# Kernel optimization log

Hardware: AMD Instinct MI355X
Metric: run time of the kernel (lower is better)

Reference implementation:

```python
import jax, jax.numpy as jnp
import numpy as np

B, K, T, H, D = 16, 49, 256, 512, 512


def setup_inputs() -> dict:
    key = jax.random.key(0)
    ks = jax.random.split(key, 8)
    s = 1.0 / np.sqrt(H)
    return {
        "V": jax.random.normal(ks[0], (B, K, H), jnp.float32),
        "h_t": jax.random.normal(ks[1], (B, T, H), jnp.float32),
        "s_t": jax.random.normal(ks[2], (B, T, H), jnp.float32),
        "Wv": jax.random.normal(ks[3], (H, D), jnp.float32) * s,
        "bv": jnp.zeros((D,), jnp.float32),
        "Wg": jax.random.normal(ks[4], (H, D), jnp.float32) * s,
        "bg": jnp.zeros((D,), jnp.float32),
        "Ws": jax.random.normal(ks[5], (H, D), jnp.float32) * s,
        "bs": jnp.zeros((D,), jnp.float32),
        "Wh": jax.random.normal(ks[6], (D, 1), jnp.float32) * (1.0 / np.sqrt(D)),
        "bh": jnp.zeros((1,), jnp.float32),
    }


def reference(V, h_t, s_t, Wv, bv, Wg, bg, Ws, bs, Wh, bh):
    # projections (dropout is identity in eval)
    cv = V @ Wv + bv                        # [B, K, D]
    cg = h_t @ Wg + bg                      # [B, T, D]
    # content_v: [B, T, K, D] via broadcast add
    content_v = cv[:, None, :, :] + cg[:, :, None, :]
    z_t = (jnp.tanh(content_v) @ Wh + bh)[..., 0]   # [B, T, K]
    alpha_t = jax.nn.softmax(z_t, axis=-1)          # [B, T, K]
    c_t = jnp.einsum('btk,bkh->bth', alpha_t, V)    # [B, T, H]
    # sentinel branch
    content_s = (s_t @ Ws + bs) + cg                # [B, T, D]
    z_ext = jnp.tanh(content_s) @ Wh + bh           # [B, T, 1]
    extended = jnp.concatenate([z_t, z_ext], axis=-1)  # [B, T, K+1]
    alpha_hat = jax.nn.softmax(extended, axis=-1)
    beta_t = alpha_hat[:, :, -1:]                   # [B, T, 1]
    c_hat_t = beta_t * s_t + (1.0 - beta_t) * c_t   # [B, T, H]
    return (c_hat_t, alpha_t, beta_t)
```

## Files before the change

kernel.cpp:

```cpp
#include <hip/hip_runtime.h>
#include <hip/hip_fp16.h>
#include <cstdint>
#include <cstddef>

#define B_ 16
#define K_ 49
#define T_ 256
#define H_ 512
#define D_ 512

#define TANH_SCALE 2.8853900817779268f
#define LOG2E 1.4426950408889634f

typedef _Float16 half8 __attribute__((ext_vector_type(8)));
typedef float floatx4 __attribute__((ext_vector_type(4)));

#define ROWS_A 9088
#define OFF_V 0
#define OFF_H 896
#define OFF_S 4992

__global__ __launch_bounds__(256) void conv_a(const float* __restrict__ V,
                                              const float* __restrict__ h_t,
                                              const float* __restrict__ s_t,
                                              _Float16* __restrict__ Af16) {
    int idx = (blockIdx.x * 256 + threadIdx.x) * 8;
    int row = idx >> 9;
    int col = idx & 511;
    const float* src;
    if (row < 784)        src = V   + (size_t)row * 512 + col;
    else if (row < 896)   src = nullptr;
    else if (row < 4992)  src = h_t + (size_t)(row - 896) * 512 + col;
    else                  src = s_t + (size_t)(row - 4992) * 512 + col;

    half8 h;
    if (src) {
        float4 f0 = *(const float4*)(src);
        float4 f1 = *(const float4*)(src + 4);
        h[0] = (_Float16)f0.x; h[1] = (_Float16)f0.y;
        h[2] = (_Float16)f0.z; h[3] = (_Float16)f0.w;
        h[4] = (_Float16)f1.x; h[5] = (_Float16)f1.y;
        h[6] = (_Float16)f1.z; h[7] = (_Float16)f1.w;
    } else {
        h = (half8)((_Float16)0.0f);
    }
    *(half8*)(Af16 + idx) = h;
}

__global__ __launch_bounds__(256) void conv_w(const float* __restrict__ Wv,
                                              const float* __restrict__ Wg,
                                              const float* __restrict__ Ws,
                                              _Float16* __restrict__ Wt) {
    int p = blockIdx.z;
    const float* W = (p == 0) ? Wv : (p == 1) ? Wg : Ws;
    _Float16* outp = Wt + (size_t)p * 512 * 512;
    __shared__ float tile[32][33];
    int tx = threadIdx.x, ty = threadIdx.y;
    int c = blockIdx.x * 32 + tx;
    int rbase = blockIdx.y * 32;
#pragma unroll
    for (int i = 0; i < 4; i++)
        tile[ty + i * 8][tx] = W[(size_t)(rbase + ty + i * 8) * 512 + c];
    __syncthreads();
    int k = rbase + tx;
#pragma unroll
    for (int i = 0; i < 4; i++) {
        int n = blockIdx.x * 32 + ty + i * 8;
        outp[(size_t)n * 512 + k] = (_Float16)(tile[tx][ty + i * 8] * TANH_SCALE);
    }
}

#define GS 56
__global__ __launch_bounds__(256) void gemm_f16(
    const _Float16* __restrict__ Af16, const _Float16* __restrict__ Wt,
    const float* __restrict__ bv, const float* __restrict__ bg2,
    const float* __restrict__ bs, float* __restrict__ cv,
    float* __restrict__ cg, float* __restrict__ cs) {
    __shared__ __align__(16) _Float16 As[128 * GS];
    __shared__ __align__(16) _Float16 Bs[128 * GS];

    int id = blockIdx.x;
    int rowbase; const _Float16* Bt; const float* bias; float* C;
    if (id < 28)        { rowbase = OFF_V; Bt = Wt;            bias = bv;  C = cv; }
    else if (id < 156)  { id -= 28;  rowbase = OFF_H; Bt = Wt + 262144; bias = bg2; C = cg; }
    else                { id -= 156; rowbase = OFF_S; Bt = Wt + 524288; bias = bs;  C = cs; }
    int tm = id >> 2, tn = id & 3;

    int tid = threadIdx.x;
    int wave = tid >> 6, lane = tid & 63;
    int wm = wave >> 1, wn = wave & 1;

    int sr = tid >> 1;
    int sc = (tid & 1) << 4;
    const _Float16* ag  = Af16 + (size_t)(rowbase + tm * 128 + sr) * 512 + sc;
    const _Float16* bgp = Bt   + (size_t)(tn * 128 + sr) * 512 + sc;
    _Float16* asw = &As[sr * GS + sc];
    _Float16* bsw = &Bs[sr * GS + sc];

    int fm = lane & 15, q = lane >> 4;
    const _Float16* ar = &As[(wm * 64 + fm) * GS + q * 8];
    const _Float16* br = &Bs[(wn * 64 + fm) * GS + q * 8];

    floatx4 acc[4][4];
#pragma unroll
    for (int x = 0; x < 4; x++)
#pragma unroll
        for (int y = 0; y < 4; y++) acc[x][y] = (floatx4)0.0f;

    for (int kk = 0; kk < 16; kk++) {
        if (kk) __syncthreads();
        int4 a0 = *(const int4*)(ag);
        int4 a1 = *(const int4*)(ag + 8);
        int4 b0 = *(const int4*)(bgp);
        int4 b1 = *(const int4*)(bgp + 8);
        ag += 32; bgp += 32;
        *(int4*)(asw)     = a0;
        *(int4*)(asw + 8) = a1;
        *(int4*)(bsw)     = b0;
        *(int4*)(bsw + 8) = b1;
        __syncthreads();

        half8 af[4], bf[4];
#pragma unroll
        for (int x = 0; x < 4; x++) af[x] = *(const half8*)(ar + x * 16 * GS);
#pragma unroll
        for (int y = 0; y < 4; y++) bf[y] = *(const half8*)(br + y * 16 * GS);
#pragma unroll
        for (int x = 0; x < 4; x++)
#pragma unroll
            for (int y = 0; y < 4; y++)
                acc[x][y] = __builtin_amdgcn_mfma_f32_16x16x32_f16(af[x], bf[y], acc[x][y], 0, 0, 0);
    }

    int dn = lane & 15, dq = lane >> 4;
#pragma unroll
    for (int x = 0; x < 4; x++) {
        int rowg = tm * 128 + wm * 64 + x * 16 + dq * 4;
#pragma unroll
        for (int y = 0; y < 4; y++) {
            int colg = tn * 128 + wn * 64 + y * 16 + dn;
            float bc = bias[colg] * TANH_SCALE;
#pragma unroll
            for (int r = 0; r < 4; r++)
                C[(size_t)(rowg + r) * 512 + colg] = acc[x][y][r] + bc;
        }
    }
}

__device__ __forceinline__ float wave_sum(float v) {
#pragma unroll
    for (int o = 32; o > 0; o >>= 1) v += __shfl_xor(v, o);
    return v;
}
__device__ __forceinline__ float wave_max(float v) {
#pragma unroll
    for (int o = 32; o > 0; o >>= 1) v = fmaxf(v, __shfl_xor(v, o));
    return v;
}

#define TB 4
__global__ __launch_bounds__(256) void z_kernel(
    const float* __restrict__ cv, const float* __restrict__ cg,
    const float* __restrict__ cs, const float* __restrict__ V,
    const float* __restrict__ s_t, const float* __restrict__ Wh,
    const float* __restrict__ bh, float* __restrict__ out) {
    int bx = blockIdx.x;
    int b  = bx >> 6;
    int t0 = (bx & 63) << 2;
    int bt0 = b * 256 + t0;
    int tid = threadIdx.x;
    int wave = tid >> 6, lane = tid & 63;

    __shared__ float zl[TB][64];
    __shared__ float4 al4[52];
    __shared__ float bl[TB];

    float whv[8], cgv[TB][8];
#pragma unroll
    for (int j = 0; j < 8; j++) whv[j] = Wh[j * 64 + lane];
#pragma unroll
    for (int tt = 0; tt < TB; tt++) {
        const float* cgp = cg + (size_t)(bt0 + tt) * 512;
#pragma unroll
        for (int j = 0; j < 8; j++) cgv[tt][j] = cgp[j * 64 + lane];
    }
    float s8 = 0.0f;
#pragma unroll
    for (int j = 0; j < 8; j++) s8 += whv[j];
    float zbase = wave_sum(s8) + bh[0];

    for (int task = wave; task < 49; task += 4) {
        const float* rp = cv + (size_t)(b * 49 + task) * 512;
        float rv[8];
#pragma unroll
        for (int j = 0; j < 8; j++) rv[j] = rp[j * 64 + lane];
        float acc[TB] = {0.0f, 0.0f, 0.0f, 0.0f};
#pragma unroll
        for (int tt = 0; tt < TB; tt++) {
#pragma unroll
            for (int j = 0; j < 8; j++) {
                float x = rv[j] + cgv[tt][j];
                float e = __builtin_amdgcn_exp2f(x);
                float r = __builtin_amdgcn_rcpf(1.0f + e);
                acc[tt] = fmaf(whv[j], r, acc[tt]);
            }
        }
#pragma unroll
        for (int tt = 0; tt < TB; tt++) {
            float s = wave_sum(acc[tt]);
            if (lane == 0) zl[tt][task] = zbase - 2.0f * s;
        }
    }
#pragma unroll
    for (int tt = 0; tt < TB; tt++) {
        if (wave == tt) {
            const float* rp = cs + (size_t)(bt0 + tt) * 512;
            float acc = 0.0f;
#pragma unroll
            for (int j = 0; j < 8; j++) {
                float x = rp[j * 64 + lane] + cgv[tt][j];
                float e = __builtin_amdgcn_exp2f(x);
                float r = __builtin_amdgcn_rcpf(1.0f + e);
                acc = fmaf(whv[j], r, acc);
            }
            float s = wave_sum(acc);
            if (lane == 0) zl[tt][49] = zbase - 2.0f * s;
        }
    }
    __syncthreads();

    {
        int w = wave;
        float z = (lane < 49) ? zl[w][lane] : -3.0e38f;
        float m = wave_max(z);
        float e = (lane < 49) ? __builtin_amdgcn_exp2f((z - m) * LOG2E) : 0.0f;
        float s = wave_sum(e);
        float zext = zl[w][49];
        float m2 = fmaxf(m, zext);
        float sc   = __builtin_amdgcn_exp2f((m - m2) * LOG2E);
        float eext = __builtin_amdgcn_exp2f((zext - m2) * LOG2E);
        float s2 = s * sc + eext;
        float beta = eext / s2;
        if (lane < 49) {
            float a = e / s;
            ((float*)&al4[lane])[w] = a;
            out[(size_t)B_ * T_ * H_ + (size_t)(bt0 + w) * 49 + lane] = a;
        }
        if (lane == 0) {
            bl[w] = beta;
            out[(size_t)B_ * T_ * H_ + (size_t)B_ * T_ * K_ + (bt0 + w)] = beta;
        }
    }
    __syncthreads();

    const float* Vb = V + (size_t)b * 49 * 512;
    float acc1[TB] = {0, 0, 0, 0}, acc2[TB] = {0, 0, 0, 0};
    for (int k = 0; k < 49; k++) {
        float4 a4 = al4[k];
        float v1 = Vb[(size_t)k * 512 + tid];
        float v2 = Vb[(size_t)k * 512 + 256 + tid];
        acc1[0] = fmaf(a4.x, v1, acc1[0]);  acc2[0] = fmaf(a4.x, v2, acc2[0]);
        acc1[1] = fmaf(a4.y, v1, acc1[1]);  acc2[1] = fmaf(a4.y, v2, acc2[1]);
        acc1[2] = fmaf(a4.z, v1, acc1[2]);  acc2[2] = fmaf(a4.z, v2, acc2[2]);
        acc1[3] = fmaf(a4.w, v1, acc1[3]);  acc2[3] = fmaf(a4.w, v2, acc2[3]);
    }
#pragma unroll
    for (int tt = 0; tt < TB; tt++) {
        float beta = bl[tt];
        const float* sp = s_t + (size_t)(bt0 + tt) * 512;
        out[(size_t)(bt0 + tt) * 512 + tid]       = beta * sp[tid]       + (1.0f - beta) * acc1[tt];
        out[(size_t)(bt0 + tt) * 512 + 256 + tid] = beta * sp[tid + 256] + (1.0f - beta) * acc2[tt];
    }
}

extern "C" void kernel_launch(void* const* d_in, const int* in_sizes, int n_in,
                              void* d_out, int out_size, void* d_ws, size_t ws_size,
                              hipStream_t stream) {
    const float* V   = (const float*)d_in[0];
    const float* h_t = (const float*)d_in[1];
    const float* s_t = (const float*)d_in[2];
    const float* Wv  = (const float*)d_in[3];
    const float* bv  = (const float*)d_in[4];
    const float* Wg  = (const float*)d_in[5];
    const float* bg  = (const float*)d_in[6];
    const float* Ws  = (const float*)d_in[7];
    const float* bs  = (const float*)d_in[8];
    const float* Wh  = (const float*)d_in[9];
    const float* bh  = (const float*)d_in[10];
    float* out = (float*)d_out;

    char* ws = (char*)d_ws;
    _Float16* Af16 = (_Float16*)(ws);
    _Float16* Wt   = (_Float16*)(ws + 9306112);
    float* cv = (float*)(ws + 10878976);
    float* cg = (float*)(ws + 12713984);
    float* cs = (float*)(ws + 21102592);

    conv_a<<<2272, 256, 0, stream>>>(V, h_t, s_t, Af16);
    conv_w<<<dim3(16, 16, 3), dim3(32, 8), 0, stream>>>(Wv, Wg, Ws, Wt);
    gemm_f16<<<284, 256, 0, stream>>>(Af16, Wt, bv, bg, bs, cv, cg, cs);
    z_kernel<<<1024, 256, 0, stream>>>(cv, cg, cs, V, s_t, Wh, bh, out);
}
```

Baseline: 143.0 us.

## Merge conversion kernels, retile GEMM with async LDS loads, overlap z_kernel loads

Folds the activation and weight fp16 conversion kernels into one launch to save a kernel launch. The GEMM moves to 64x128 tiles with twice as many blocks, loads K=64 per stage through global_load_lds into a pre-swizzled fragment layout, and each wave now covers a 64x32 output slice. In z_kernel the next cv row is prefetched into registers, the four per-row wave reductions are replaced by a combined butterfly reduction, and the alpha·V loop is unrolled. Smaller tiles raise occupancy across CUs but reduce data reuse per block.

Result: no change. 140.6 us (-1.7%).

```diff
diff --git a/kernel.cpp b/kernel.cpp
--- a/kernel.cpp
+++ b/kernel.cpp
@@ -20,125 +20,141 @@
 #define OFF_H 896
 #define OFF_S 4992
 
-__global__ __launch_bounds__(256) void conv_a(const float* __restrict__ V,
-                                              const float* __restrict__ h_t,
-                                              const float* __restrict__ s_t,
-                                              _Float16* __restrict__ Af16) {
-    int idx = (blockIdx.x * 256 + threadIdx.x) * 8;
-    int row = idx >> 9;
-    int col = idx & 511;
-    const float* src;
-    if (row < 784)        src = V   + (size_t)row * 512 + col;
-    else if (row < 896)   src = nullptr;
-    else if (row < 4992)  src = h_t + (size_t)(row - 896) * 512 + col;
-    else                  src = s_t + (size_t)(row - 4992) * 512 + col;
-
-    half8 h;
-    if (src) {
-        float4 f0 = *(const float4*)(src);
-        float4 f1 = *(const float4*)(src + 4);
-        h[0] = (_Float16)f0.x; h[1] = (_Float16)f0.y;
-        h[2] = (_Float16)f0.z; h[3] = (_Float16)f0.w;
-        h[4] = (_Float16)f1.x; h[5] = (_Float16)f1.y;
-        h[6] = (_Float16)f1.z; h[7] = (_Float16)f1.w;
+__device__ __forceinline__ void async16(const _Float16* g, const _Float16* l) {
+    __builtin_amdgcn_global_load_lds(
+        (const __attribute__((address_space(1))) unsigned int*)g,
+        (__attribute__((address_space(3))) unsigned int*)l, 16, 0, 0);
+}
+
+__global__ __launch_bounds__(256) void conv_all(const float* __restrict__ V,
+                                                const float* __restrict__ h_t,
+                                                const float* __restrict__ s_t,
+                                                const float* __restrict__ Wv,
+                                                const float* __restrict__ Wg,
+                                                const float* __restrict__ Ws,
+                                                _Float16* __restrict__ Af16,
+                                                _Float16* __restrict__ Wt) {
+    __shared__ float tile[32][33];
+    int tid = threadIdx.x;
+    if (blockIdx.x < 2272) {
+        int idx = (blockIdx.x * 256 + tid) * 8;
+        int row = idx >> 9;
+        int col = idx & 511;
+        const float* src;
+        if (row < 784)        src = V   + (size_t)row * 512 + col;
+        else if (row < 896)   src = nullptr;
+        else if (row < 4992)  src = h_t + (size_t)(row - 896) * 512 + col;
+        else                  src = s_t + (size_t)(row - 4992) * 512 + col;
+        half8 h;
+        if (src) {
+            float4 f0 = *(const float4*)(src);
+            float4 f1 = *(const float4*)(src + 4);
+            h[0] = (_Float16)f0.x; h[1] = (_Float16)f0.y;
+            h[2] = (_Float16)f0.z; h[3] = (_Float16)f0.w;
+            h[4] = (_Float16)f1.x; h[5] = (_Float16)f1.y;
+            h[6] = (_Float16)f1.z; h[7] = (_Float16)f1.w;
+        } else {
+            h = (half8)((_Float16)0.0f);
+        }
+        *(half8*)(Af16 + idx) = h;
     } else {
-        h = (half8)((_Float16)0.0f);
-    }
-    *(half8*)(Af16 + idx) = h;
-}
-
-__global__ __launch_bounds__(256) void conv_w(const float* __restrict__ Wv,
-                                              const float* __restrict__ Wg,
-                                              const float* __restrict__ Ws,
-                                              _Float16* __restrict__ Wt) {
-    int p = blockIdx.z;
-    const float* W = (p == 0) ? Wv : (p == 1) ? Wg : Ws;
-    _Float16* outp = Wt + (size_t)p * 512 * 512;
-    __shared__ float tile[32][33];
-    int tx = threadIdx.x, ty = threadIdx.y;
-    int c = blockIdx.x * 32 + tx;
-    int rbase = blockIdx.y * 32;
-#pragma unroll
-    for (int i = 0; i < 4; i++)
-        tile[ty + i * 8][tx] = W[(size_t)(rbase + ty + i * 8) * 512 + c];
-    __syncthreads();
-    int k = rbase + tx;
-#pragma unroll
-    for (int i = 0; i < 4; i++) {
-        int n = blockIdx.x * 32 + ty + i * 8;
-        outp[(size_t)n * 512 + k] = (_Float16)(tile[tx][ty + i * 8] * TANH_SCALE);
-    }
-}
-
-#define GS 56
+        int bid = blockIdx.x - 2272;
+        int p = bid >> 8;
+        int rem = bid & 255;
+        int bx = rem & 15, by = rem >> 4;
+        const float* W = (p == 0) ? Wv : (p == 1) ? Wg : Ws;
+        _Float16* outp = Wt + (size_t)p * 512 * 512;
+        int tx = tid & 31, ty = tid >> 5;
+        int c = bx * 32 + tx;
+        int rbase = by * 32;
+#pragma unroll
+        for (int i = 0; i < 4; i++)
+            tile[ty + i * 8][tx] = W[(size_t)(rbase + ty + i * 8) * 512 + c];
+        __syncthreads();
+        int k = rbase + tx;
+#pragma unroll
+        for (int i = 0; i < 4; i++) {
+            int n = bx * 32 + ty + i * 8;
+            outp[(size_t)n * 512 + k] = (_Float16)(tile[tx][ty + i * 8] * TANH_SCALE);
+        }
+    }
+}
+
 __global__ __launch_bounds__(256) void gemm_f16(
     const _Float16* __restrict__ Af16, const _Float16* __restrict__ Wt,
     const float* __restrict__ bv, const float* __restrict__ bg2,
     const float* __restrict__ bs, float* __restrict__ cv,
     float* __restrict__ cg, float* __restrict__ cs) {
-    __shared__ __align__(16) _Float16 As[128 * GS];
-    __shared__ __align__(16) _Float16 Bs[128 * GS];
+    __shared__ __align__(16) _Float16 As[64 * 64];
+    __shared__ __align__(16) _Float16 Bs[128 * 64];
 
     int id = blockIdx.x;
     int rowbase; const _Float16* Bt; const float* bias; float* C;
-    if (id < 28)        { rowbase = OFF_V; Bt = Wt;            bias = bv;  C = cv; }
-    else if (id < 156)  { id -= 28;  rowbase = OFF_H; Bt = Wt + 262144; bias = bg2; C = cg; }
-    else                { id -= 156; rowbase = OFF_S; Bt = Wt + 524288; bias = bs;  C = cs; }
+    if (id < 56)        { rowbase = OFF_V;            Bt = Wt;          bias = bv;  C = cv; }
+    else if (id < 312)  { id -= 56;  rowbase = OFF_H; Bt = Wt + 262144; bias = bg2; C = cg; }
+    else                { id -= 312; rowbase = OFF_S; Bt = Wt + 524288; bias = bs;  C = cs; }
     int tm = id >> 2, tn = id & 3;
 
     int tid = threadIdx.x;
     int wave = tid >> 6, lane = tid & 63;
-    int wm = wave >> 1, wn = wave & 1;
-
-    int sr = tid >> 1;
-    int sc = (tid & 1) << 4;
-    const _Float16* ag  = Af16 + (size_t)(rowbase + tm * 128 + sr) * 512 + sc;
-    const _Float16* bgp = Bt   + (size_t)(tn * 128 + sr) * 512 + sc;
-    _Float16* asw = &As[sr * GS + sc];
-    _Float16* bsw = &Bs[sr * GS + sc];
-
-    int fm = lane & 15, q = lane >> 4;
-    const _Float16* ar = &As[(wm * 64 + fm) * GS + q * 8];
-    const _Float16* br = &Bs[(wn * 64 + fm) * GS + q * 8];
-
-    floatx4 acc[4][4];
+
+    const _Float16* gA[2];
+    int ldsA[2];
+#pragma unroll
+    for (int i = 0; i < 2; i++) {
+        int p = i * 256 + tid;
+        int ks = p >> 8, x = (p >> 6) & 3, q = (p >> 4) & 3, fm = p & 15;
+        gA[i] = Af16 + (size_t)(rowbase + tm * 64 + x * 16 + fm) * 512 + ks * 32 + q * 8;
+        ldsA[i] = p * 8;
+    }
+    const _Float16* gB[4];
+    int ldsB[4];
+#pragma unroll
+    for (int i = 0; i < 4; i++) {
+        int p = i * 256 + tid;
+        int ks = p >> 9, w2y = (p >> 6) & 7, q = (p >> 4) & 3, fn = p & 15;
+        gB[i] = Bt + (size_t)(tn * 128 + w2y * 16 + fn) * 512 + ks * 32 + q * 8;
+        ldsB[i] = p * 8;
+    }
+
+    floatx4 acc[4][2];
 #pragma unroll
     for (int x = 0; x < 4; x++)
 #pragma unroll
-        for (int y = 0; y < 4; y++) acc[x][y] = (floatx4)0.0f;
-
-    for (int kk = 0; kk < 16; kk++) {
+        for (int y = 0; y < 2; y++) acc[x][y] = (floatx4)0.0f;
+
+    for (int kk = 0; kk < 8; kk++) {
         if (kk) __syncthreads();
-        int4 a0 = *(const int4*)(ag);
-        int4 a1 = *(const int4*)(ag + 8);
-        int4 b0 = *(const int4*)(bgp);
-        int4 b1 = *(const int4*)(bgp + 8);
-        ag += 32; bgp += 32;
-        *(int4*)(asw)     = a0;
-        *(int4*)(asw + 8) = a1;
-        *(int4*)(bsw)     = b0;
-        *(int4*)(bsw + 8) = b1;
+#pragma unroll
+        for (int i = 0; i < 2; i++) async16(gA[i] + kk * 64, &As[ldsA[i]]);
+#pragma unroll
+        for (int i = 0; i < 4; i++) async16(gB[i] + kk * 64, &Bs[ldsB[i]]);
         __syncthreads();
 
-        half8 af[4], bf[4];
-#pragma unroll
-        for (int x = 0; x < 4; x++) af[x] = *(const half8*)(ar + x * 16 * GS);
-#pragma unroll
-        for (int y = 0; y < 4; y++) bf[y] = *(const half8*)(br + y * 16 * GS);
-#pragma unroll
-        for (int x = 0; x < 4; x++)
-#pragma unroll
-            for (int y = 0; y < 4; y++)
-                acc[x][y] = __builtin_amdgcn_mfma_f32_16x16x32_f16(af[x], bf[y], acc[x][y], 0, 0, 0);
+#pragma unroll
+        for (int ks = 0; ks < 2; ks++) {
+            half8 a[4], bf[2];
+#pragma unroll
+            for (int x = 0; x < 4; x++)
+                a[x] = *(const half8*)&As[((ks * 4 + x) * 64 + lane) * 8];
+#pragma unroll
+            for (int y = 0; y < 2; y++)
+                bf[y] = *(const half8*)&Bs[((ks * 8 + wave * 2 + y) * 64 + lane) * 8];
+#pragma unroll
+            for (int x = 0; x < 4; x++)
+#pragma unroll
+                for (int y = 0; y < 2; y++)
+                    acc[x][y] = __builtin_amdgcn_mfma_f32_16x16x32_f16(a[x], bf[y], acc[x][y], 0, 0, 0);
+        }
     }
 
     int dn = lane & 15, dq = lane >> 4;
 #pragma unroll
     for (int x = 0; x < 4; x++) {
-        int rowg = tm * 128 + wm * 64 + x * 16 + dq * 4;
-#pragma unroll
-        for (int y = 0; y < 4; y++) {
-            int colg = tn * 128 + wn * 64 + y * 16 + dn;
+        int rowg = tm * 64 + x * 16 + dq * 4;
+#pragma unroll
+        for (int y = 0; y < 2; y++) {
+            int colg = tn * 128 + wave * 32 + y * 16 + dn;
             float bc = bias[colg] * TANH_SCALE;
 #pragma unroll
             for (int r = 0; r < 4; r++)
@@ -156,6 +172,25 @@
 #pragma unroll
     for (int o = 32; o > 0; o >>= 1) v = fmaxf(v, __shfl_xor(v, o));
     return v;
+}
+
+__device__ __forceinline__ float xsum4(float a0, float a1, float a2, float a3, int lane) {
+    bool hi = (lane & 32) != 0;
+    float t0 = hi ? a0 : a2;
+    float t1 = hi ? a1 : a3;
+    t0 = __shfl_xor(t0, 32);
+    t1 = __shfl_xor(t1, 32);
+    if (hi) { a0 = t0; a1 = t1; } else { a2 = t0; a3 = t1; }
+    bool h2 = (lane & 16) != 0;
+    float u0 = h2 ? a0 : a1;
+    float u1 = h2 ? a2 : a3;
+    u0 = __shfl_xor(u0, 16);
+    u1 = __shfl_xor(u1, 16);
+    if (h2) { a0 = u0; a2 = u1; } else { a1 = u0; a3 = u1; }
+    float s = (a0 + a1) + (a2 + a3);
+#pragma unroll
+    for (int o = 8; o > 0; o >>= 1) s += __shfl_xor(s, o);
+    return s;
 }
 
 #define TB 4
@@ -189,11 +224,19 @@
     for (int j = 0; j < 8; j++) s8 += whv[j];
     float zbase = wave_sum(s8) + bh[0];
 
+    float rv[8], rn[8];
+    {
+        const float* rp = cv + (size_t)(b * 49 + wave) * 512;
+#pragma unroll
+        for (int j = 0; j < 8; j++) rv[j] = rp[j * 64 + lane];
+    }
     for (int task = wave; task < 49; task += 4) {
-        const float* rp = cv + (size_t)(b * 49 + task) * 512;
-        float rv[8];
-#pragma unroll
-        for (int j = 0; j < 8; j++) rv[j] = rp[j * 64 + lane];
+        int nt = task + 4;
+        if (nt < 49) {
+            const float* rp = cv + (size_t)(b * 49 + nt) * 512;
+#pragma unroll
+            for (int j = 0; j < 8; j++) rn[j] = rp[j * 64 + lane];
+        }
         float acc[TB] = {0.0f, 0.0f, 0.0f, 0.0f};
 #pragma unroll
         for (int tt = 0; tt < TB; tt++) {
@@ -205,11 +248,10 @@
                 acc[tt] = fmaf(whv[j], r, acc[tt]);
             }
         }
-#pragma unroll
-        for (int tt = 0; tt < TB; tt++) {
-            float s = wave_sum(acc[tt]);
-            if (lane == 0) zl[tt][task] = zbase - 2.0f * s;
-        }
+        float z = xsum4(acc[0], acc[1], acc[2], acc[3], lane);
+        if ((lane & 15) == 0) zl[lane >> 4][task] = zbase - 2.0f * z;
+#pragma unroll
+        for (int j = 0; j < 8; j++) rv[j] = rn[j];
     }
 #pragma unroll
     for (int tt = 0; tt < TB; tt++) {
@@ -255,6 +297,7 @@
 
     const float* Vb = V + (size_t)b * 49 * 512;
     float acc1[TB] = {0, 0, 0, 0}, acc2[TB] = {0, 0, 0, 0};
+#pragma unroll 7
     for (int k = 0; k < 49; k++) {
         float4 a4 = al4[k];
         float v1 = Vb[(size_t)k * 512 + tid];
@@ -296,8 +339,7 @@
     float* cg = (float*)(ws + 12713984);
     float* cs = (float*)(ws + 21102592);
 
-    conv_a<<<2272, 256, 0, stream>>>(V, h_t, s_t, Af16);
-    conv_w<<<dim3(16, 16, 3), dim3(32, 8), 0, stream>>>(Wv, Wg, Ws, Wt);
-    gemm_f16<<<284, 256, 0, stream>>>(Af16, Wt, bv, bg, bs, cv, cg, cs);
+    conv_all<<<3040, 256, 0, stream>>>(V, h_t, s_t, Wv, Wg, Ws, Af16, Wt);
+    gemm_f16<<<568, 256, 0, stream>>>(Af16, Wt, bv, bg, bs, cv, cg, cs);
     z_kernel<<<1024, 256, 0, stream>>>(cv, cg, cs, V, s_t, Wh, bh, out);
 }
```
